# Optimization experiments

Measured on AMD Instinct MI355X. Metric: run time of the kernel, lower is better.

## Reference

```python
import jax, jax.numpy as jnp
import numpy as np

B = 32768
D_IN = 512
D_OUT = 512
N_DIGITS = 9
N_LEVELS = N_DIGITS + 1


def _xavier_uniform(key, shape, gain):
    # nn.init.xavier_uniform_ on Linear weight of shape (out, in)
    fan_out, fan_in = shape
    limit = gain * np.sqrt(6.0 / (fan_in + fan_out))
    return jax.random.uniform(key, shape, jnp.float32, -limit, limit)


def setup_inputs() -> dict:
    key = jax.random.key(0)
    kx, kv, *kw = jax.random.split(key, 2 + N_LEVELS)
    x = jax.random.normal(kx, (B, D_IN), dtype=jnp.float32)
    valuations = jax.random.randint(kv, (B,), 0, N_LEVELS, dtype=jnp.int64)
    # level-aware xavier init: gain = 1/(1 + 0.1*level)
    W = jnp.stack([
        _xavier_uniform(kw[l], (D_OUT, D_IN), 1.0 / (1.0 + 0.1 * l))
        for l in range(N_LEVELS)
    ], axis=0)  # (L, out, in)
    level_gates = jnp.ones((N_LEVELS,), dtype=jnp.float32)
    cross_level_attn = (jnp.eye(N_LEVELS, dtype=jnp.float32) * 0.9
                        + jnp.ones((N_LEVELS, N_LEVELS), dtype=jnp.float32) * 0.01)
    bias = jnp.zeros((D_OUT,), dtype=jnp.float32)
    return {"x": x, "valuations": valuations, "W": W,
            "level_gates": level_gates, "cross_level_attn": cross_level_attn,
            "bias": bias}


def reference(x, valuations, W, level_gates, cross_level_attn, bias):
    val = jnp.clip(valuations, 0, N_DIGITS)  # (B,)
    # 10 per-level linears as one batched GEMM: (B, L, out)
    level_outputs = jnp.einsum('bi,loi->blo', x, W)
    gates = jax.nn.sigmoid(level_gates)  # (L,)
    level_outputs = level_outputs * gates[None, :, None]
    # per-sample gather of own valuation level -> (B, out)
    output = jnp.take_along_axis(level_outputs, val[:, None, None], axis=1)[:, 0, :]
    # soft cross-level attention combine
    attn_weights = jax.nn.softmax(cross_level_attn[val], axis=-1)  # (B, L)
    weighted = jnp.einsum('bl,blo->bo', attn_weights, level_outputs)
    output = 0.7 * output + 0.3 * weighted
    return output + bias
```

## Files before the change

### kernel.cpp

```cpp
#include <hip/hip_runtime.h>

#define B_N 32768
#define D 512
#define NLEV 10
#define TM 128
#define TN 128
#define BK 32
#define MROWS_MAX 34048
#define MAX_RT (MROWS_MAX / TM)

typedef unsigned short u16;
typedef short s16x8 __attribute__((ext_vector_type(8)));
typedef u16 u16x8 __attribute__((ext_vector_type(8)));
typedef float f32x4 __attribute__((ext_vector_type(4)));

__device__ __forceinline__ u16 f2bf(float f) {
  union { float f; unsigned u; } v; v.f = f;
  unsigned r = v.u + 0x7fffu + ((v.u >> 16) & 1u);
  return (u16)(r >> 16);
}


__global__ void k_prep(const float* __restrict__ lg, const float* __restrict__ attn,
                       float* __restrict__ coef, int* __restrict__ counts) {
  int t = threadIdx.x;
  if (t < NLEV) {
    float g[NLEV], a[NLEV];
    float mx = -1e30f;
    #pragma unroll
    for (int l = 0; l < NLEV; ++l) {
      g[l] = 1.0f / (1.0f + expf(-lg[l]));
      a[l] = attn[t * NLEV + l];
      mx = fmaxf(mx, a[l]);
    }
    float s = 0.0f;
    #pragma unroll
    for (int l = 0; l < NLEV; ++l) { a[l] = expf(a[l] - mx); s += a[l]; }
    float inv = 1.0f / s;
    #pragma unroll
    for (int l = 0; l < NLEV; ++l) {
      float c = 0.3f * a[l] * inv * g[l];
      if (l == t) c += 0.7f * g[t];
      coef[t * NLEV + l] = c;
    }
  }
  if (t >= 32 && t < 32 + NLEV) counts[t - 32] = 0;
}

__global__ void k_hist(const int* __restrict__ val, int* __restrict__ counts,
                       int* __restrict__ perm) {
  __shared__ int lc[NLEV];
  int t = threadIdx.x;
  int gid = blockIdx.x * 256 + t;
  if (t < NLEV) lc[t] = 0;
  __syncthreads();
  if (gid < B_N) {
    int v = val[gid]; v = v < 0 ? 0 : (v > NLEV - 1 ? NLEV - 1 : v);
    atomicAdd(&lc[v], 1);
  }
  if (gid < MROWS_MAX) perm[gid] = -1;
  __syncthreads();
  if (t < NLEV && lc[t] > 0) atomicAdd(&counts[t], lc[t]);
}

__global__ void k_scan(const int* __restrict__ counts, int* __restrict__ starts,
                       int* __restrict__ cursors) {
  if (threadIdx.x == 0 && blockIdx.x == 0) {
    int s = 0;
    for (int v = 0; v < NLEV; ++v) {
      starts[v] = s;
      cursors[v] = s;
      s += (counts[v] + TM - 1) & ~(TM - 1);
    }
    starts[NLEV] = s;
  }
}

__global__ void k_scatter(const int* __restrict__ val, int* __restrict__ cursors,
                          int* __restrict__ perm) {
  __shared__ int bcnt[NLEV], base[NLEV];
  int t = threadIdx.x;
  int gid = blockIdx.x * 256 + t;
  if (t < NLEV) bcnt[t] = 0;
  __syncthreads();
  int v = -1, pos = 0;
  if (gid < B_N) {
    v = val[gid]; v = v < 0 ? 0 : (v > NLEV - 1 ? NLEV - 1 : v);
    pos = atomicAdd(&bcnt[v], 1);
  }
  __syncthreads();
  if (t < NLEV && bcnt[t] > 0) base[t] = atomicAdd(&cursors[t], bcnt[t]);
  __syncthreads();
  if (v >= 0) perm[base[v] + pos] = gid;
}

__global__ void k_weff(const float* __restrict__ W, const float* __restrict__ coef,
                       u16* __restrict__ weff) {
  __shared__ float c[NLEV * NLEV];
  int t = threadIdx.x;
  if (t < NLEV * NLEV) c[t] = coef[t];
  __syncthreads();
  int idx = blockIdx.x * 256 + t;
  float w[NLEV];
  #pragma unroll
  for (int l = 0; l < NLEV; ++l) w[l] = W[l * (D * D) + idx];
  #pragma unroll
  for (int v = 0; v < NLEV; ++v) {
    float s = 0.0f;
    #pragma unroll
    for (int l = 0; l < NLEV; ++l) s += c[v * NLEV + l] * w[l];
    weff[v * (D * D) + idx] = f2bf(s);
  }
}

__global__ __launch_bounds__(256, 2) void k_gemm(
    const float* __restrict__ x, const u16* __restrict__ weff,
    const int* __restrict__ perm, const int* __restrict__ starts,
    const float* __restrict__ bias, float* __restrict__ out) {
  __shared__ u16 As[TM * BK];
  __shared__ u16 Bs[TN * BK];

  const int rt = blockIdx.y, ct = blockIdx.x;
  const int Mpad = starts[NLEV];
  if (rt * TM >= Mpad) return;

  int v = 0;
  #pragma unroll
  for (int i = 1; i < NLEV; ++i) if (rt * TM >= starts[i]) v = i;

  const int tid = threadIdx.x;
  const int lane = tid & 63, wave = tid >> 6;
  const int wm = (wave >> 1) * 64, wn = (wave & 1) * 64;
  const int fm = lane & 15;
  const int cb = lane >> 4;

  const int ar = tid >> 1;
  const int ah = tid & 1;
  int prow = perm[rt * TM + ar];
  if (prow < 0) prow = 0;
  const float* xrow = x + (size_t)prow * D + ah * 16;
  const int sw = (ar >> 1) & 3;

  const u16* wb = weff + ((size_t)v * D + ct * TN) * D;

  f32x4 acc[4][4];
  #pragma unroll
  for (int i = 0; i < 4; ++i)
    #pragma unroll
    for (int j = 0; j < 4; ++j) acc[i][j] = (f32x4){0.f, 0.f, 0.f, 0.f};

  for (int k0 = 0; k0 < D; k0 += BK) {
    #pragma unroll
    for (int j = 0; j < 2; ++j) {
      int c = j * 256 + wave * 64 + lane;
      int n_ = c >> 2, kc = c & 3;
      const u16* g = wb + n_ * D + k0 + kc * 8;
      __builtin_amdgcn_global_load_lds(
          (const __attribute__((address_space(1))) void*)g,
          (__attribute__((address_space(3))) void*)(Bs + (j * 256 + wave * 64) * 8),
          16, 0, 0);
    }
    const f32x4* xp = (const f32x4*)(xrow + k0);
    f32x4 f0 = xp[0], f1 = xp[1], f2 = xp[2], f3 = xp[3];
    u16x8 c0, c1;
    #pragma unroll
    for (int q = 0; q < 4; ++q) {
      c0[q] = f2bf(f0[q]); c0[4 + q] = f2bf(f1[q]);
      c1[q] = f2bf(f2[q]); c1[4 + q] = f2bf(f3[q]);
    }
    *(u16x8*)(As + ar * BK + (((ah * 2 + 0) ^ sw) << 3)) = c0;
    *(u16x8*)(As + ar * BK + (((ah * 2 + 1) ^ sw) << 3)) = c1;
    __syncthreads();

    s16x8 af[4], bf[4];
    #pragma unroll
    for (int t = 0; t < 4; ++t) {
      int m = wm + t * 16 + fm;
      af[t] = *(const s16x8*)(As + m * BK + ((cb ^ ((m >> 1) & 3)) << 3));
      int n = wn + t * 16 + fm;
      bf[t] = *(const s16x8*)(Bs + n * BK + (cb << 3));
    }
    #pragma unroll
    for (int tm = 0; tm < 4; ++tm)
      #pragma unroll
      for (int tn = 0; tn < 4; ++tn)
        acc[tm][tn] = __builtin_amdgcn_mfma_f32_16x16x32_bf16(af[tm], bf[tn], acc[tm][tn], 0, 0, 0);
    __syncthreads();
  }

  float bv[4];
  #pragma unroll
  for (int tn = 0; tn < 4; ++tn) bv[tn] = bias[ct * TN + wn + tn * 16 + fm];
  #pragma unroll
  for (int tm = 0; tm < 4; ++tm) {
    #pragma unroll
    for (int r = 0; r < 4; ++r) {
      int mrow = wm + tm * 16 + (lane >> 4) * 4 + r;
      int p = perm[rt * TM + mrow];
      if (p >= 0) {
        float* o = out + (size_t)p * D + ct * TN + wn + fm;
        #pragma unroll
        for (int tn = 0; tn < 4; ++tn)
          o[tn * 16] = acc[tm][tn][r] + bv[tn];
      }
    }
  }
}


__global__ __launch_bounds__(256, 2) void k_gemm_folded(
    const float* __restrict__ x, const int* __restrict__ val,
    const float* __restrict__ W, const float* __restrict__ lg,
    const float* __restrict__ attn, const float* __restrict__ bias,
    float* __restrict__ out) {
  __shared__ u16 As[TM * BK];
  __shared__ u16 Bs[TN * BK];
  __shared__ float cf[NLEV * NLEV];

  const int tid = threadIdx.x;
  if (tid < NLEV) {
    float g[NLEV], a[NLEV];
    float mx = -1e30f;
    #pragma unroll
    for (int l = 0; l < NLEV; ++l) {
      g[l] = 1.0f / (1.0f + expf(-lg[l]));
      a[l] = attn[tid * NLEV + l];
      mx = fmaxf(mx, a[l]);
    }
    float s = 0.0f;
    #pragma unroll
    for (int l = 0; l < NLEV; ++l) { a[l] = expf(a[l] - mx); s += a[l]; }
    float inv = 1.0f / s;
    #pragma unroll
    for (int l = 0; l < NLEV; ++l) {
      float c = 0.3f * a[l] * inv * g[l];
      if (l == tid) c += 0.7f * g[tid];
      cf[tid * NLEV + l] = c;
    }
  }

  const int ct = blockIdx.x, mt = blockIdx.y;
  const int lane = tid & 63, wave = tid >> 6;
  const int wm = (wave >> 1) * 64, wn = (wave & 1) * 64;
  const int fm = lane & 15;
  const int cb = lane >> 4;
  const int ar = tid >> 1, ah = tid & 1;
  const int sw = (ar >> 1) & 3;

  const float* xrow = x + (size_t)(mt * TM + ar) * D + ah * 16;
  const float* wrow = W + (size_t)(ct * TN + ar) * D + ah * 16;
  int v = val[mt * TM + ar];
  v = v < 0 ? 0 : (v > NLEV - 1 ? NLEV - 1 : v);
  __syncthreads();

  f32x4 acc[4][4];
  #pragma unroll
  for (int i = 0; i < 4; ++i)
    #pragma unroll
    for (int j = 0; j < 4; ++j) acc[i][j] = (f32x4){0.f, 0.f, 0.f, 0.f};

  for (int l = 0; l < NLEV; ++l) {
    const float sc = cf[v * NLEV + l];
    const float* wl = wrow + (size_t)l * D * D;
    for (int kk = 0; kk < D; kk += BK) {
      const f32x4* xp = (const f32x4*)(xrow + kk);
      f32x4 f0 = xp[0], f1 = xp[1], f2 = xp[2], f3 = xp[3];
      u16x8 c0, c1;
      #pragma unroll
      for (int q = 0; q < 4; ++q) {
        c0[q] = f2bf(sc * f0[q]); c0[4 + q] = f2bf(sc * f1[q]);
        c1[q] = f2bf(sc * f2[q]); c1[4 + q] = f2bf(sc * f3[q]);
      }
      *(u16x8*)(As + ar * BK + (((ah * 2 + 0) ^ sw) << 3)) = c0;
      *(u16x8*)(As + ar * BK + (((ah * 2 + 1) ^ sw) << 3)) = c1;
      const f32x4* wp = (const f32x4*)(wl + kk);
      f32x4 g0 = wp[0], g1 = wp[1], g2 = wp[2], g3 = wp[3];
      u16x8 d0, d1;
      #pragma unroll
      for (int q = 0; q < 4; ++q) {
        d0[q] = f2bf(g0[q]); d0[4 + q] = f2bf(g1[q]);
        d1[q] = f2bf(g2[q]); d1[4 + q] = f2bf(g3[q]);
      }
      *(u16x8*)(Bs + ar * BK + (((ah * 2 + 0) ^ sw) << 3)) = d0;
      *(u16x8*)(Bs + ar * BK + (((ah * 2 + 1) ^ sw) << 3)) = d1;
      __syncthreads();

      s16x8 af[4], bf[4];
      #pragma unroll
      for (int t = 0; t < 4; ++t) {
        int m = wm + t * 16 + fm;
        af[t] = *(const s16x8*)(As + m * BK + ((cb ^ ((m >> 1) & 3)) << 3));
        int n = wn + t * 16 + fm;
        bf[t] = *(const s16x8*)(Bs + n * BK + ((cb ^ ((n >> 1) & 3)) << 3));
      }
      #pragma unroll
      for (int tm = 0; tm < 4; ++tm)
        #pragma unroll
        for (int tn = 0; tn < 4; ++tn)
          acc[tm][tn] = __builtin_amdgcn_mfma_f32_16x16x32_bf16(af[tm], bf[tn], acc[tm][tn], 0, 0, 0);
      __syncthreads();
    }
  }

  float bv[4];
  #pragma unroll
  for (int tn = 0; tn < 4; ++tn) bv[tn] = bias[ct * TN + wn + tn * 16 + fm];
  #pragma unroll
  for (int tm = 0; tm < 4; ++tm) {
    #pragma unroll
    for (int r = 0; r < 4; ++r) {
      int mrow = mt * TM + wm + tm * 16 + (lane >> 4) * 4 + r;
      float* o = out + (size_t)mrow * D + ct * TN + wn + fm;
      #pragma unroll
      for (int tn = 0; tn < 4; ++tn)
        o[tn * 16] = acc[tm][tn][r] + bv[tn];
    }
  }
}

extern "C" void kernel_launch(void* const* d_in, const int* in_sizes, int n_in,
                              void* d_out, int out_size, void* d_ws, size_t ws_size,
                              hipStream_t stream) {
  const float* x    = (const float*)d_in[0];
  const int*   val  = (const int*)d_in[1];
  const float* W    = (const float*)d_in[2];
  const float* lg   = (const float*)d_in[3];
  const float* attn = (const float*)d_in[4];
  const float* bias = (const float*)d_in[5];
  float* out = (float*)d_out;

  const size_t REQ = 139264 + (size_t)NLEV * D * D * 2;

  if (d_ws != nullptr && ws_size >= REQ) {
    char* ws = (char*)d_ws;
    float* coef  = (float*)(ws + 0);
    int* counts  = (int*)(ws + 512);
    int* starts  = (int*)(ws + 1024);
    int* cursors = (int*)(ws + 1536);
    int* perm    = (int*)(ws + 2048);
    u16* weff    = (u16*)(ws + 139264);

    k_prep<<<1, 64, 0, stream>>>(lg, attn, coef, counts);
    k_hist<<<MROWS_MAX / 256, 256, 0, stream>>>(val, counts, perm);
    k_scan<<<1, 64, 0, stream>>>(counts, starts, cursors);
    k_scatter<<<B_N / 256, 256, 0, stream>>>(val, cursors, perm);
    k_weff<<<(D * D) / 256, 256, 0, stream>>>(W, coef, weff);
    k_gemm<<<dim3(D / TN, MAX_RT), 256, 0, stream>>>(x, weff, perm, starts, bias, out);
  } else {
    k_gemm_folded<<<dim3(D / TN, B_N / TM), 256, 0, stream>>>(
        x, val, W, lg, attn, bias, out);
  }
}
```

Before: 192.5 us.

## Fuse prep kernels into three launches and widen GEMM tile to 256 columns

The six-kernel pipeline becomes three launches. The first kernel computes W_eff in some blocks and per-block level histograms in others. The second does a deterministic prefix-sum scatter with no global atomics. The GEMM now uses 512 threads with a 128x256 tile, so each x row is loaded and converted to bf16 half as many times. The B tile gets an XOR-swizzled LDS layout to cut bank conflicts, and the folded fallback path and workspace-size check are removed. This trades launch and serialization overhead for larger blocks, which may lower occupancy, and the workspace is now assumed to exist.

```diff
diff --git a/kernel.cpp b/kernel.cpp
--- a/kernel.cpp
+++ b/kernel.cpp
@@ -2,10 +2,12 @@
 
 #define B_N 32768
 #define D 512
+#define DD (D * D)
 #define NLEV 10
 #define TM 128
-#define TN 128
+#define TN 256
 #define BK 32
+#define NHB 128
 #define MROWS_MAX 34048
 #define MAX_RT (MROWS_MAX / TM)
 
@@ -19,108 +21,106 @@
   unsigned r = v.u + 0x7fffu + ((v.u >> 16) & 1u);
   return (u16)(r >> 16);
 }
-
-
-__global__ void k_prep(const float* __restrict__ lg, const float* __restrict__ attn,
-                       float* __restrict__ coef, int* __restrict__ counts) {
-  int t = threadIdx.x;
-  if (t < NLEV) {
-    float g[NLEV], a[NLEV];
-    float mx = -1e30f;
-    #pragma unroll
-    for (int l = 0; l < NLEV; ++l) {
-      g[l] = 1.0f / (1.0f + expf(-lg[l]));
-      a[l] = attn[t * NLEV + l];
-      mx = fmaxf(mx, a[l]);
-    }
-    float s = 0.0f;
-    #pragma unroll
-    for (int l = 0; l < NLEV; ++l) { a[l] = expf(a[l] - mx); s += a[l]; }
-    float inv = 1.0f / s;
-    #pragma unroll
-    for (int l = 0; l < NLEV; ++l) {
-      float c = 0.3f * a[l] * inv * g[l];
-      if (l == t) c += 0.7f * g[t];
-      coef[t * NLEV + l] = c;
-    }
-  }
-  if (t >= 32 && t < 32 + NLEV) counts[t - 32] = 0;
-}
-
-__global__ void k_hist(const int* __restrict__ val, int* __restrict__ counts,
-                       int* __restrict__ perm) {
+__device__ __forceinline__ int clampv(int v) {
+  return v < 0 ? 0 : (v > NLEV - 1 ? NLEV - 1 : v);
+}
+
+__global__ void k1(const float* __restrict__ W, const float* __restrict__ lg,
+                   const float* __restrict__ attn, const int* __restrict__ val,
+                   u16* __restrict__ weff, u16* __restrict__ hist,
+                   int* __restrict__ perm) {
+  const int t = threadIdx.x;
+  if (blockIdx.x < DD / 256) {
+    __shared__ float c[NLEV * NLEV];
+    if (t < NLEV) {
+      float g[NLEV], a[NLEV], mx = -1e30f;
+      #pragma unroll
+      for (int l = 0; l < NLEV; ++l) {
+        g[l] = 1.0f / (1.0f + expf(-lg[l]));
+        a[l] = attn[t * NLEV + l];
+        mx = fmaxf(mx, a[l]);
+      }
+      float s = 0.f;
+      #pragma unroll
+      for (int l = 0; l < NLEV; ++l) { a[l] = expf(a[l] - mx); s += a[l]; }
+      float inv = 1.0f / s;
+      #pragma unroll
+      for (int l = 0; l < NLEV; ++l) {
+        float cc = 0.3f * a[l] * inv * g[l];
+        if (l == t) cc += 0.7f * g[t];
+        c[t * NLEV + l] = cc;
+      }
+    }
+    __syncthreads();
+    const int idx = blockIdx.x * 256 + t;
+    float w[NLEV];
+    #pragma unroll
+    for (int l = 0; l < NLEV; ++l) w[l] = W[l * DD + idx];
+    #pragma unroll
+    for (int v = 0; v < NLEV; ++v) {
+      float s = 0.f;
+      #pragma unroll
+      for (int l = 0; l < NLEV; ++l) s += c[v * NLEV + l] * w[l];
+      weff[v * DD + idx] = f2bf(s);
+    }
+  } else {
+    __shared__ int lc[NLEV];
+    const int b = blockIdx.x - DD / 256;
+    if (t < NLEV) lc[t] = 0;
+    __syncthreads();
+    const int gid = b * 256 + t;
+    atomicAdd(&lc[clampv(val[gid])], 1);
+    perm[gid] = -1;
+    if (b < (MROWS_MAX - B_N) / 256) perm[B_N + b * 256 + t] = -1;
+    __syncthreads();
+    if (t < NLEV) hist[b * NLEV + t] = (u16)lc[t];
+  }
+}
+
+__global__ void k2(const int* __restrict__ val, const u16* __restrict__ hist,
+                   int* __restrict__ perm, int* __restrict__ starts) {
+  __shared__ int h[NHB * NLEV];
+  __shared__ int st[NLEV + 1];
+  __shared__ int cnt[NLEV];
   __shared__ int lc[NLEV];
-  int t = threadIdx.x;
-  int gid = blockIdx.x * 256 + t;
+  const int t = threadIdx.x, b = blockIdx.x;
+  for (int i = t; i < NHB * NLEV; i += 256) h[i] = hist[i];
   if (t < NLEV) lc[t] = 0;
   __syncthreads();
-  if (gid < B_N) {
-    int v = val[gid]; v = v < 0 ? 0 : (v > NLEV - 1 ? NLEV - 1 : v);
-    atomicAdd(&lc[v], 1);
-  }
-  if (gid < MROWS_MAX) perm[gid] = -1;
+  if (t < NLEV) {
+    int run = 0;
+    for (int bb = 0; bb < NHB; ++bb) {
+      int x = h[bb * NLEV + t];
+      h[bb * NLEV + t] = run;
+      run += x;
+    }
+    cnt[t] = run;
+  }
   __syncthreads();
-  if (t < NLEV && lc[t] > 0) atomicAdd(&counts[t], lc[t]);
-}
-
-__global__ void k_scan(const int* __restrict__ counts, int* __restrict__ starts,
-                       int* __restrict__ cursors) {
-  if (threadIdx.x == 0 && blockIdx.x == 0) {
+  if (t == 0) {
     int s = 0;
     for (int v = 0; v < NLEV; ++v) {
-      starts[v] = s;
-      cursors[v] = s;
-      s += (counts[v] + TM - 1) & ~(TM - 1);
-    }
-    starts[NLEV] = s;
-  }
-}
-
-__global__ void k_scatter(const int* __restrict__ val, int* __restrict__ cursors,
-                          int* __restrict__ perm) {
-  __shared__ int bcnt[NLEV], base[NLEV];
-  int t = threadIdx.x;
-  int gid = blockIdx.x * 256 + t;
-  if (t < NLEV) bcnt[t] = 0;
+      st[v] = s;
+      s += (cnt[v] + TM - 1) & ~(TM - 1);
+    }
+    st[NLEV] = s;
+  }
   __syncthreads();
-  int v = -1, pos = 0;
-  if (gid < B_N) {
-    v = val[gid]; v = v < 0 ? 0 : (v > NLEV - 1 ? NLEV - 1 : v);
-    pos = atomicAdd(&bcnt[v], 1);
-  }
-  __syncthreads();
-  if (t < NLEV && bcnt[t] > 0) base[t] = atomicAdd(&cursors[t], bcnt[t]);
-  __syncthreads();
-  if (v >= 0) perm[base[v] + pos] = gid;
-}
-
-__global__ void k_weff(const float* __restrict__ W, const float* __restrict__ coef,
-                       u16* __restrict__ weff) {
-  __shared__ float c[NLEV * NLEV];
-  int t = threadIdx.x;
-  if (t < NLEV * NLEV) c[t] = coef[t];
-  __syncthreads();
-  int idx = blockIdx.x * 256 + t;
-  float w[NLEV];
-  #pragma unroll
-  for (int l = 0; l < NLEV; ++l) w[l] = W[l * (D * D) + idx];
-  #pragma unroll
-  for (int v = 0; v < NLEV; ++v) {
-    float s = 0.0f;
-    #pragma unroll
-    for (int l = 0; l < NLEV; ++l) s += c[v * NLEV + l] * w[l];
-    weff[v * (D * D) + idx] = f2bf(s);
-  }
-}
-
-__global__ __launch_bounds__(256, 2) void k_gemm(
+  const int gid = b * 256 + t;
+  const int v = clampv(val[gid]);
+  const int pos = atomicAdd(&lc[v], 1);
+  perm[st[v] + h[b * NLEV + v] + pos] = gid;
+  if (b == 0 && t <= NLEV) starts[t] = st[t];
+}
+
+__global__ __launch_bounds__(512, 4) void k3(
     const float* __restrict__ x, const u16* __restrict__ weff,
     const int* __restrict__ perm, const int* __restrict__ starts,
     const float* __restrict__ bias, float* __restrict__ out) {
   __shared__ u16 As[TM * BK];
   __shared__ u16 Bs[TN * BK];
 
-  const int rt = blockIdx.y, ct = blockIdx.x;
+  const int ct = blockIdx.x, rt = blockIdx.y;
   const int Mpad = starts[NLEV];
   if (rt * TM >= Mpad) return;
 
@@ -130,15 +130,15 @@
 
   const int tid = threadIdx.x;
   const int lane = tid & 63, wave = tid >> 6;
-  const int wm = (wave >> 1) * 64, wn = (wave & 1) * 64;
+  const int wm = (wave >> 2) * 64, wn = (wave & 3) * 64;
   const int fm = lane & 15;
   const int cb = lane >> 4;
 
-  const int ar = tid >> 1;
-  const int ah = tid & 1;
+  const int ar = tid >> 2;
+  const int ah = tid & 3;
   int prow = perm[rt * TM + ar];
   if (prow < 0) prow = 0;
-  const float* xrow = x + (size_t)prow * D + ah * 16;
+  const float* xrow = x + (size_t)prow * D + ah * 8;
   const int sw = (ar >> 1) & 3;
 
   const u16* wb = weff + ((size_t)v * D + ct * TN) * D;
@@ -152,33 +152,30 @@
   for (int k0 = 0; k0 < D; k0 += BK) {
     #pragma unroll
     for (int j = 0; j < 2; ++j) {
-      int c = j * 256 + wave * 64 + lane;
-      int n_ = c >> 2, kc = c & 3;
+      const int c = j * 512 + wave * 64 + lane;
+      const int n_ = c >> 2, slot = c & 3;
+      const int kc = slot ^ ((n_ >> 1) & 3);
       const u16* g = wb + n_ * D + k0 + kc * 8;
       __builtin_amdgcn_global_load_lds(
           (const __attribute__((address_space(1))) void*)g,
-          (__attribute__((address_space(3))) void*)(Bs + (j * 256 + wave * 64) * 8),
+          (__attribute__((address_space(3))) void*)(Bs + (j * 512 + wave * 64) * 8),
           16, 0, 0);
     }
     const f32x4* xp = (const f32x4*)(xrow + k0);
-    f32x4 f0 = xp[0], f1 = xp[1], f2 = xp[2], f3 = xp[3];
-    u16x8 c0, c1;
-    #pragma unroll
-    for (int q = 0; q < 4; ++q) {
-      c0[q] = f2bf(f0[q]); c0[4 + q] = f2bf(f1[q]);
-      c1[q] = f2bf(f2[q]); c1[4 + q] = f2bf(f3[q]);
-    }
-    *(u16x8*)(As + ar * BK + (((ah * 2 + 0) ^ sw) << 3)) = c0;
-    *(u16x8*)(As + ar * BK + (((ah * 2 + 1) ^ sw) << 3)) = c1;
+    f32x4 f0 = xp[0], f1 = xp[1];
+    u16x8 c0;
+    #pragma unroll
+    for (int q = 0; q < 4; ++q) { c0[q] = f2bf(f0[q]); c0[4 + q] = f2bf(f1[q]); }
+    *(u16x8*)(As + ar * BK + ((ah ^ sw) << 3)) = c0;
     __syncthreads();
 
     s16x8 af[4], bf[4];
     #pragma unroll
-    for (int t = 0; t < 4; ++t) {
-      int m = wm + t * 16 + fm;
-      af[t] = *(const s16x8*)(As + m * BK + ((cb ^ ((m >> 1) & 3)) << 3));
-      int n = wn + t * 16 + fm;
-      bf[t] = *(const s16x8*)(Bs + n * BK + (cb << 3));
+    for (int t4 = 0; t4 < 4; ++t4) {
+      const int m = wm + t4 * 16 + fm;
+      af[t4] = *(const s16x8*)(As + m * BK + ((cb ^ ((m >> 1) & 3)) << 3));
+      const int n = wn + t4 * 16 + fm;
+      bf[t4] = *(const s16x8*)(Bs + n * BK + ((cb ^ ((n >> 1) & 3)) << 3));
     }
     #pragma unroll
     for (int tm = 0; tm < 4; ++tm)
@@ -195,125 +192,14 @@
   for (int tm = 0; tm < 4; ++tm) {
     #pragma unroll
     for (int r = 0; r < 4; ++r) {
-      int mrow = wm + tm * 16 + (lane >> 4) * 4 + r;
-      int p = perm[rt * TM + mrow];
+      const int mrow = wm + tm * 16 + (lane >> 4) * 4 + r;
+      const int p = perm[rt * TM + mrow];
       if (p >= 0) {
         float* o = out + (size_t)p * D + ct * TN + wn + fm;
         #pragma unroll
         for (int tn = 0; tn < 4; ++tn)
           o[tn * 16] = acc[tm][tn][r] + bv[tn];
       }
-    }
-  }
-}
-
-
-__global__ __launch_bounds__(256, 2) void k_gemm_folded(
-    const float* __restrict__ x, const int* __restrict__ val,
-    const float* __restrict__ W, const float* __restrict__ lg,
-    const float* __restrict__ attn, const float* __restrict__ bias,
-    float* __restrict__ out) {
-  __shared__ u16 As[TM * BK];
-  __shared__ u16 Bs[TN * BK];
-  __shared__ float cf[NLEV * NLEV];
-
-  const int tid = threadIdx.x;
-  if (tid < NLEV) {
-    float g[NLEV], a[NLEV];
-    float mx = -1e30f;
-    #pragma unroll
-    for (int l = 0; l < NLEV; ++l) {
-      g[l] = 1.0f / (1.0f + expf(-lg[l]));
-      a[l] = attn[tid * NLEV + l];
-      mx = fmaxf(mx, a[l]);
-    }
-    float s = 0.0f;
-    #pragma unroll
-    for (int l = 0; l < NLEV; ++l) { a[l] = expf(a[l] - mx); s += a[l]; }
-    float inv = 1.0f / s;
-    #pragma unroll
-    for (int l = 0; l < NLEV; ++l) {
-      float c = 0.3f * a[l] * inv * g[l];
-      if (l == tid) c += 0.7f * g[tid];
-      cf[tid * NLEV + l] = c;
-    }
-  }
-
-  const int ct = blockIdx.x, mt = blockIdx.y;
-  const int lane = tid & 63, wave = tid >> 6;
-  const int wm = (wave >> 1) * 64, wn = (wave & 1) * 64;
-  const int fm = lane & 15;
-  const int cb = lane >> 4;
-  const int ar = tid >> 1, ah = tid & 1;
-  const int sw = (ar >> 1) & 3;
-
-  const float* xrow = x + (size_t)(mt * TM + ar) * D + ah * 16;
-  const float* wrow = W + (size_t)(ct * TN + ar) * D + ah * 16;
-  int v = val[mt * TM + ar];
-  v = v < 0 ? 0 : (v > NLEV - 1 ? NLEV - 1 : v);
-  __syncthreads();
-
-  f32x4 acc[4][4];
-  #pragma unroll
-  for (int i = 0; i < 4; ++i)
-    #pragma unroll
-    for (int j = 0; j < 4; ++j) acc[i][j] = (f32x4){0.f, 0.f, 0.f, 0.f};
-
-  for (int l = 0; l < NLEV; ++l) {
-    const float sc = cf[v * NLEV + l];
-    const float* wl = wrow + (size_t)l * D * D;
-    for (int kk = 0; kk < D; kk += BK) {
-      const f32x4* xp = (const f32x4*)(xrow + kk);
-      f32x4 f0 = xp[0], f1 = xp[1], f2 = xp[2], f3 = xp[3];
-      u16x8 c0, c1;
-      #pragma unroll
-      for (int q = 0; q < 4; ++q) {
-        c0[q] = f2bf(sc * f0[q]); c0[4 + q] = f2bf(sc * f1[q]);
-        c1[q] = f2bf(sc * f2[q]); c1[4 + q] = f2bf(sc * f3[q]);
-      }
-      *(u16x8*)(As + ar * BK + (((ah * 2 + 0) ^ sw) << 3)) = c0;
-      *(u16x8*)(As + ar * BK + (((ah * 2 + 1) ^ sw) << 3)) = c1;
-      const f32x4* wp = (const f32x4*)(wl + kk);
-      f32x4 g0 = wp[0], g1 = wp[1], g2 = wp[2], g3 = wp[3];
-      u16x8 d0, d1;
-      #pragma unroll
-      for (int q = 0; q < 4; ++q) {
-        d0[q] = f2bf(g0[q]); d0[4 + q] = f2bf(g1[q]);
-        d1[q] = f2bf(g2[q]); d1[4 + q] = f2bf(g3[q]);
-      }
-      *(u16x8*)(Bs + ar * BK + (((ah * 2 + 0) ^ sw) << 3)) = d0;
-      *(u16x8*)(Bs + ar * BK + (((ah * 2 + 1) ^ sw) << 3)) = d1;
-      __syncthreads();
-
-      s16x8 af[4], bf[4];
-      #pragma unroll
-      for (int t = 0; t < 4; ++t) {
-        int m = wm + t * 16 + fm;
-        af[t] = *(const s16x8*)(As + m * BK + ((cb ^ ((m >> 1) & 3)) << 3));
-        int n = wn + t * 16 + fm;
-        bf[t] = *(const s16x8*)(Bs + n * BK + ((cb ^ ((n >> 1) & 3)) << 3));
-      }
-      #pragma unroll
-      for (int tm = 0; tm < 4; ++tm)
-        #pragma unroll
-        for (int tn = 0; tn < 4; ++tn)
-          acc[tm][tn] = __builtin_amdgcn_mfma_f32_16x16x32_bf16(af[tm], bf[tn], acc[tm][tn], 0, 0, 0);
-      __syncthreads();
-    }
-  }
-
-  float bv[4];
-  #pragma unroll
-  for (int tn = 0; tn < 4; ++tn) bv[tn] = bias[ct * TN + wn + tn * 16 + fm];
-  #pragma unroll
-  for (int tm = 0; tm < 4; ++tm) {
-    #pragma unroll
-    for (int r = 0; r < 4; ++r) {
-      int mrow = mt * TM + wm + tm * 16 + (lane >> 4) * 4 + r;
-      float* o = out + (size_t)mrow * D + ct * TN + wn + fm;
-      #pragma unroll
-      for (int tn = 0; tn < 4; ++tn)
-        o[tn * 16] = acc[tm][tn][r] + bv[tn];
     }
   }
 }
@@ -329,25 +215,13 @@
   const float* bias = (const float*)d_in[5];
   float* out = (float*)d_out;
 
-  const size_t REQ = 139264 + (size_t)NLEV * D * D * 2;
-
-  if (d_ws != nullptr && ws_size >= REQ) {
-    char* ws = (char*)d_ws;
-    float* coef  = (float*)(ws + 0);
-    int* counts  = (int*)(ws + 512);
-    int* starts  = (int*)(ws + 1024);
-    int* cursors = (int*)(ws + 1536);
-    int* perm    = (int*)(ws + 2048);
-    u16* weff    = (u16*)(ws + 139264);
-
-    k_prep<<<1, 64, 0, stream>>>(lg, attn, coef, counts);
-    k_hist<<<MROWS_MAX / 256, 256, 0, stream>>>(val, counts, perm);
-    k_scan<<<1, 64, 0, stream>>>(counts, starts, cursors);
-    k_scatter<<<B_N / 256, 256, 0, stream>>>(val, cursors, perm);
-    k_weff<<<(D * D) / 256, 256, 0, stream>>>(W, coef, weff);
-    k_gemm<<<dim3(D / TN, MAX_RT), 256, 0, stream>>>(x, weff, perm, starts, bias, out);
-  } else {
-    k_gemm_folded<<<dim3(D / TN, B_N / TM), 256, 0, stream>>>(
-        x, val, W, lg, attn, bias, out);
-  }
-}
+  char* ws = (char*)d_ws;
+  int* starts = (int*)(ws + 0);
+  u16* hist   = (u16*)(ws + 64);
+  int* perm   = (int*)(ws + 2688);
+  u16* weff   = (u16*)(ws + 139264);
+
+  k1<<<DD / 256 + NHB, 256, 0, stream>>>(W, lg, attn, val, weff, hist, perm);
+  k2<<<NHB, 256, 0, stream>>>(val, hist, perm, starts);
+  k3<<<dim3(D / TN, MAX_RT), 512, 0, stream>>>(x, weff, perm, starts, bias, out);
+}
```

Result: faster. 179.2 us (-6.9%).
